# Performance work log

Measured on AMD Instinct MI355X. Metric: run time of the kernel, lower is better.

The kernel has to match this reference:

```python
import jax, jax.numpy as jnp
import numpy as np

B, S, ENC, DEC, ATT = 32, 2048, 1024, 1024, 1024


def setup_inputs() -> dict:
    key = jax.random.key(0)
    k1, k2, k3, k4, k5, k6 = jax.random.split(key, 6)
    sc = lambda fan_in: 1.0 / np.sqrt(fan_in)
    return {
        "encoder_hidden_states": jax.random.normal(k1, (B, S, ENC), dtype=jnp.float32),
        "decoder_hidden_state": jax.random.normal(k2, (B, 1, DEC), dtype=jnp.float32),
        # nn.Linear stores weight as [out, in]; we keep [in, out] for x @ W
        "U_a": jax.random.uniform(k3, (ENC, ATT), jnp.float32, -sc(ENC), sc(ENC)),
        "W_a": jax.random.uniform(k4, (DEC, ATT), jnp.float32, -sc(DEC), sc(DEC)),
        "v_t": jax.random.uniform(k5, (ATT, 1), jnp.float32, -sc(ATT), sc(ATT)),
        "ffn": jax.random.uniform(k6, (ENC + DEC, DEC), jnp.float32, -sc(ENC + DEC), sc(ENC + DEC)),
    }


def reference(encoder_hidden_states, decoder_hidden_state, U_a, W_a, v_t, ffn):
    # additive (Bahdanau) attention
    u = jnp.einsum('bse,ea->bsa', encoder_hidden_states, U_a)      # [B,S,A]
    w = jnp.einsum('bqd,da->bqa', decoder_hidden_state, W_a)       # [B,1,A]
    e = jnp.tanh(w + u) @ v_t                                      # [B,S,1]
    align = jax.nn.softmax(e, axis=1)                              # softmax over seq
    # context = alignment^T @ encoder_states  -> [B,1,E]
    context = jnp.einsum('bsq,bse->bqe', align, encoder_hidden_states)
    cat = jnp.concatenate([decoder_hidden_state, context], axis=-1)  # [B,1,D+E]
    output = jnp.tanh(cat @ ffn)                                     # [B,1,D]
    return (output, context)
```

## Files before the change

### kernel.cpp

```cpp
#include <hip/hip_runtime.h>
#include <hip/hip_bf16.h>
#include <cstdint>
#include <cstddef>

#define B_  32
#define S_  2048
#define E_  1024
#define A_  1024
#define D_  1024
#define M_TOT (B_ * S_)

typedef __attribute__((ext_vector_type(8))) __bf16 bf16x8;
typedef __attribute__((ext_vector_type(4))) float  f32x4;

__device__ __forceinline__ float fast_tanh(float x) {
    float cx = fminf(fmaxf(x, -15.f), 15.f);
    float e2 = __expf(2.f * cx);
    return 1.f - 2.f / (e2 + 1.f);
}

__device__ __forceinline__ bf16x8 cvt8(const float* __restrict__ p) {
    float4 f0 = *(const float4*)p;
    float4 f1 = *(const float4*)(p + 4);
    bf16x8 r;
    r[0] = (__bf16)f0.x; r[1] = (__bf16)f0.y; r[2] = (__bf16)f0.z; r[3] = (__bf16)f0.w;
    r[4] = (__bf16)f1.x; r[5] = (__bf16)f1.y; r[6] = (__bf16)f1.z; r[7] = (__bf16)f1.w;
    return r;
}

typedef __attribute__((address_space(3))) uint32_t lds_u32_t;
typedef __attribute__((address_space(1))) const uint32_t gbl_u32_t;
__device__ __forceinline__ void async_ld16(const void* g, void* l) {
    __builtin_amdgcn_global_load_lds((gbl_u32_t*)g,
                                     (lds_u32_t*)(uint32_t)(uintptr_t)l,
                                     16, 0, 0);
}

__global__ __launch_bounds__(256) void k_convert_enc(const float* __restrict__ enc,
                                                     __bf16* __restrict__ xb) {
    size_t idx = ((size_t)blockIdx.x * 256 + threadIdx.x) * 8;
    *(bf16x8*)(xb + idx) = cvt8(enc + idx);
}

__global__ __launch_bounds__(256) void k_trans_U(const float* __restrict__ Ua,
                                                 __bf16* __restrict__ Ut) {
    __shared__ float tile[64][65];
    int bid = blockIdx.x;
    int k0 = (bid >> 4) * 64, n0 = (bid & 15) * 64;
    int t = threadIdx.x;
    int r = t >> 6, c = t & 63;
    #pragma unroll
    for (int i = 0; i < 16; ++i)
        tile[i * 4 + r][c] = Ua[(size_t)(k0 + i * 4 + r) * 1024 + n0 + c];
    __syncthreads();
    #pragma unroll
    for (int i = 0; i < 16; ++i)
        Ut[(size_t)(n0 + i * 4 + r) * 1024 + k0 + c] = (__bf16)tile[c][i * 4 + r];
}

__global__ __launch_bounds__(256) void k_w_part(const float* __restrict__ dec,
                                                const float* __restrict__ Wa,
                                                float* __restrict__ w_part) {
    int bid = blockIdx.x;
    int ac = bid & 3, b = (bid >> 2) & 31, kc = bid >> 7;
    int a = ac * 256 + threadIdx.x;
    int k0 = kc * 128;
    float acc = 0.f;
    #pragma unroll 8
    for (int k = 0; k < 128; ++k)
        acc += dec[b * 1024 + k0 + k] * Wa[(size_t)(k0 + k) * 1024 + a];
    w_part[kc * 32768 + b * 1024 + a] = acc;
}

template <bool USE_XB>
__global__ __launch_bounds__(256) void k_gemm_e(
        const float* __restrict__ enc, const __bf16* __restrict__ Xb,
        const __bf16* __restrict__ Ut, const float* __restrict__ w_part,
        const float* __restrict__ v, float* __restrict__ e_part) {
    __shared__ __bf16 lX[2][128 * 32];
    __shared__ __bf16 lU[2][128 * 32];
    __shared__ float  e_lds[2][128];

    const int t = threadIdx.x;
    const int bid = blockIdx.x;
    const int xcd = bid & 7;
    const int j_  = bid >> 3;
    const int m_tile = xcd * 64 + (j_ >> 3);
    const int n_tile = j_ & 7;
    const int m0 = m_tile * 128;
    const int n0 = n_tile * 128;
    const int wave = t >> 6;
    const int lane = t & 63;
    const int q = lane >> 4;
    const int c = lane & 15;
    const int wm = (wave >> 1) * 64;
    const int wn = (wave & 1) * 64;

    f32x4 acc[4][4];
    #pragma unroll
    for (int i = 0; i < 4; ++i)
        #pragma unroll
        for (int j = 0; j < 4; ++j)
            #pragma unroll
            for (int r = 0; r < 4; ++r) acc[i][j][r] = 0.f;

    const int lrow = lane >> 2;
    const int lcol = (lane & 3) * 8;
    const int xrow = wave * 32;

    if (USE_XB) {
        const __bf16* gxb = Xb + (size_t)(m0 + xrow + lrow) * 1024 + lcol;
        const __bf16* gub = Ut + (size_t)(n0 + xrow + lrow) * 1024 + lcol;

        auto stage = [&](int kk, int bsel) {
            async_ld16(gxb + kk,             &lX[bsel][xrow * 32]);
            async_ld16(gxb + kk + 16 * 1024, &lX[bsel][(xrow + 16) * 32]);
            async_ld16(gub + kk,             &lU[bsel][xrow * 32]);
            async_ld16(gub + kk + 16 * 1024, &lU[bsel][(xrow + 16) * 32]);
        };
        auto compute = [&](int bsel) {
            bf16x8 af[4], bfr[4];
            #pragma unroll
            for (int i = 0; i < 4; ++i)
                af[i] = *(const bf16x8*)(&lX[bsel][(wm + i * 16 + c) * 32 + q * 8]);
            #pragma unroll
            for (int j = 0; j < 4; ++j)
                bfr[j] = *(const bf16x8*)(&lU[bsel][(wn + j * 16 + c) * 32 + q * 8]);
            #pragma unroll
            for (int i = 0; i < 4; ++i)
                #pragma unroll
                for (int j = 0; j < 4; ++j)
                    acc[i][j] = __builtin_amdgcn_mfma_f32_16x16x32_bf16(af[i], bfr[j], acc[i][j], 0, 0, 0);
        };

        stage(0, 0);
        __syncthreads();
        for (int kk = 0; kk < 1024; kk += 64) {
            if (kk + 32 < 1024) stage(kk + 32, 1);
            compute(0);
            __syncthreads();
            if (kk + 64 < 1024) stage(kk + 64, 0);
            compute(1);
            __syncthreads();
        }
    } else {
        const int srow = t >> 2;
        const int scol = (t & 3) * 8;
        for (int kk = 0; kk < 1024; kk += 32) {
            __syncthreads();
            const float* s0 = enc + (size_t)(m0 + srow) * 1024 + kk + scol;
            *(bf16x8*)(&lX[0][srow * 32])        = cvt8(s0);
            *(bf16x8*)(&lX[0][(srow + 64) * 32]) = cvt8(s0 + (size_t)64 * 1024);
            const __bf16* u0 = Ut + (size_t)(n0 + srow) * 1024 + kk + scol;
            *(int4*)(&lU[0][srow * 32])        = *(const int4*)u0;
            *(int4*)(&lU[0][(srow + 64) * 32]) = *(const int4*)(u0 + 64 * 1024);
            __syncthreads();
            bf16x8 af[4], bfr[4];
            #pragma unroll
            for (int i = 0; i < 4; ++i)
                af[i] = *(const bf16x8*)(&lX[0][(wm + i * 16 + c) * 32 + q * 8]);
            #pragma unroll
            for (int j = 0; j < 4; ++j)
                bfr[j] = *(const bf16x8*)(&lU[0][(wn + j * 16 + c) * 32 + q * 8]);
            #pragma unroll
            for (int i = 0; i < 4; ++i)
                #pragma unroll
                for (int j = 0; j < 4; ++j)
                    acc[i][j] = __builtin_amdgcn_mfma_f32_16x16x32_bf16(af[i], bfr[j], acc[i][j], 0, 0, 0);
        }
    }

    const int b_idx = m0 >> 11;
    float wv[4], vv[4];
    #pragma unroll
    for (int j = 0; j < 4; ++j) {
        int col = n0 + wn + j * 16 + c;
        float s = 0.f;
        #pragma unroll
        for (int p = 0; p < 8; ++p) s += w_part[p * 32768 + b_idx * 1024 + col];
        wv[j] = s;
        vv[j] = v[col];
    }
    #pragma unroll
    for (int i = 0; i < 4; ++i) {
        float s0 = 0.f, s1 = 0.f, s2 = 0.f, s3 = 0.f;
        #pragma unroll
        for (int j = 0; j < 4; ++j) {
            s0 += fast_tanh(wv[j] + acc[i][j][0]) * vv[j];
            s1 += fast_tanh(wv[j] + acc[i][j][1]) * vv[j];
            s2 += fast_tanh(wv[j] + acc[i][j][2]) * vv[j];
            s3 += fast_tanh(wv[j] + acc[i][j][3]) * vv[j];
        }
        #pragma unroll
        for (int off = 1; off < 16; off <<= 1) {
            s0 += __shfl_xor(s0, off, 16);
            s1 += __shfl_xor(s1, off, 16);
            s2 += __shfl_xor(s2, off, 16);
            s3 += __shfl_xor(s3, off, 16);
        }
        if (c == 0) {
            int row = wm + i * 16 + q * 4;
            e_lds[wave & 1][row + 0] = s0;
            e_lds[wave & 1][row + 1] = s1;
            e_lds[wave & 1][row + 2] = s2;
            e_lds[wave & 1][row + 3] = s3;
        }
    }
    __syncthreads();
    if (t < 128)
        e_part[(size_t)n_tile * M_TOT + m0 + t] = e_lds[0][t] + e_lds[1][t];
}

__global__ __launch_bounds__(256) void k_softmax(const float* __restrict__ ep,
                                                 float* __restrict__ al) {
    int b = blockIdx.x, t = threadIdx.x;
    float ev[8];
    #pragma unroll
    for (int i = 0; i < 8; ++i) {
        int s = i * 256 + t;
        float x = 0.f;
        #pragma unroll
        for (int p = 0; p < 8; ++p) x += ep[p * M_TOT + b * 2048 + s];
        ev[i] = x;
    }
    float mx = ev[0];
    #pragma unroll
    for (int i = 1; i < 8; ++i) mx = fmaxf(mx, ev[i]);
    #pragma unroll
    for (int off = 1; off < 64; off <<= 1) mx = fmaxf(mx, __shfl_xor(mx, off, 64));
    __shared__ float redm[4];
    if ((t & 63) == 0) redm[t >> 6] = mx;
    __syncthreads();
    mx = fmaxf(fmaxf(redm[0], redm[1]), fmaxf(redm[2], redm[3]));

    float ex[8], sm = 0.f;
    #pragma unroll
    for (int i = 0; i < 8; ++i) { ex[i] = __expf(ev[i] - mx); sm += ex[i]; }
    #pragma unroll
    for (int off = 1; off < 64; off <<= 1) sm += __shfl_xor(sm, off, 64);
    __shared__ float reds[4];
    if ((t & 63) == 0) reds[t >> 6] = sm;
    __syncthreads();
    sm = reds[0] + reds[1] + reds[2] + reds[3];
    float inv = 1.f / sm;
    #pragma unroll
    for (int i = 0; i < 8; ++i) al[b * 2048 + i * 256 + t] = ex[i] * inv;
}

template <bool USE_XB>
__global__ __launch_bounds__(256) void k_ctx(const float* __restrict__ enc,
                                             const __bf16* __restrict__ Xb,
                                             const float* __restrict__ al,
                                             float* __restrict__ ctx_part) {
    int b  = blockIdx.x >> 5;
    int sc = blockIdx.x & 31;
    int t  = threadIdx.x;
    int sh = t >> 7;
    int e8 = (t & 127) * 8;
    float acc[8];
    #pragma unroll
    for (int r = 0; r < 8; ++r) acc[r] = 0.f;
    int rbase = sc * 64 + sh * 32;
    for (int i = 0; i < 32; i += 4) {
        #pragma unroll
        for (int u = 0; u < 4; ++u) {
            int s = rbase + i + u;
            float a = al[b * 2048 + s];
            if (USE_XB) {
                bf16x8 x = *(const bf16x8*)(Xb + (size_t)(b * 2048 + s) * 1024 + e8);
                #pragma unroll
                for (int r = 0; r < 8; ++r) acc[r] += a * (float)x[r];
            } else {
                const float* xp = enc + (size_t)(b * 2048 + s) * 1024 + e8;
                float4 x0 = *(const float4*)xp;
                float4 x1 = *(const float4*)(xp + 4);
                acc[0] += a * x0.x; acc[1] += a * x0.y; acc[2] += a * x0.z; acc[3] += a * x0.w;
                acc[4] += a * x1.x; acc[5] += a * x1.y; acc[6] += a * x1.z; acc[7] += a * x1.w;
            }
        }
    }
    float* o = ctx_part + ((size_t)(sc * 2 + sh) * 32 + b) * 1024 + e8;
    float4 r0; r0.x = acc[0]; r0.y = acc[1]; r0.z = acc[2]; r0.w = acc[3];
    float4 r1; r1.x = acc[4]; r1.y = acc[5]; r1.z = acc[6]; r1.w = acc[7];
    *(float4*)o = r0;
    *(float4*)(o + 4) = r1;
}

__global__ __launch_bounds__(256) void k_ctx_sum(const float* __restrict__ ctx_part,
                                                 float* __restrict__ ctx,
                                                 float* __restrict__ out) {
    int idx = blockIdx.x * 256 + threadIdx.x;
    float s = 0.f;
    #pragma unroll
    for (int p = 0; p < 64; ++p) s += ctx_part[(size_t)p * 32768 + idx];
    ctx[idx] = s;
    out[32768 + idx] = s;
}

__global__ __launch_bounds__(256) void k_out_part(const float* __restrict__ dec,
                                                  const float* __restrict__ ctx,
                                                  const float* __restrict__ ffn,
                                                  float* __restrict__ out_part) {
    int bid = blockIdx.x;
    int b = bid & 31, kc = bid >> 5;
    int t = threadIdx.x;
    __shared__ float catl[256];
    int i0 = kc * 256;
    catl[t] = (i0 < 1024) ? dec[b * 1024 + i0 + t] : ctx[b * 1024 + i0 - 1024 + t];
    __syncthreads();
    float a0 = 0.f, a1 = 0.f, a2 = 0.f, a3 = 0.f;
    #pragma unroll 4
    for (int i = 0; i < 256; ++i) {
        float cv = catl[i];
        const float* fr = ffn + (size_t)(i0 + i) * 1024;
        a0 += cv * fr[t];
        a1 += cv * fr[t + 256];
        a2 += cv * fr[t + 512];
        a3 += cv * fr[t + 768];
    }
    float* o = out_part + ((size_t)kc * 32 + b) * 1024;
    o[t] = a0; o[t + 256] = a1; o[t + 512] = a2; o[t + 768] = a3;
}

__global__ __launch_bounds__(256) void k_out_final(const float* __restrict__ out_part,
                                                   float* __restrict__ out) {
    int idx = blockIdx.x * 256 + threadIdx.x;
    float s = 0.f;
    #pragma unroll
    for (int p = 0; p < 8; ++p) s += out_part[(size_t)p * 32768 + idx];
    out[idx] = fast_tanh(s);
}

extern "C" void kernel_launch(void* const* d_in, const int* in_sizes, int n_in,
                              void* d_out, int out_size, void* d_ws, size_t ws_size,
                              hipStream_t stream) {
    const float* enc = (const float*)d_in[0];
    const float* dec = (const float*)d_in[1];
    const float* Ua  = (const float*)d_in[2];
    const float* Wa  = (const float*)d_in[3];
    const float* vt  = (const float*)d_in[4];
    const float* ffn = (const float*)d_in[5];
    float* out = (float*)d_out;

    char* ws = (char*)d_ws;
    size_t off = 0;
    __bf16* Ut       = (__bf16*)(ws + off); off += (size_t)A_ * E_ * 2;
    float*  e_part   = (float*)(ws + off);  off += (size_t)8 * M_TOT * 4;
    float*  al       = (float*)(ws + off);  off += (size_t)M_TOT * 4;
    float*  w_part   = (float*)(ws + off);  off += (size_t)8 * B_ * 1024 * 4;
    float*  ctx_part = (float*)(ws + off);  off += (size_t)64 * B_ * 1024 * 4;
    float*  ctx      = (float*)(ws + off);  off += (size_t)B_ * 1024 * 4;
    float*  out_part = (float*)(ws + off);  off += (size_t)8 * B_ * 1024 * 4;
    off = (off + 255) & ~(size_t)255;
    __bf16* Xb       = (__bf16*)(ws + off);
    bool use_xb = (ws_size >= off + (size_t)M_TOT * E_ * 2);

    if (use_xb)
        k_convert_enc<<<(M_TOT * E_) / (256 * 8), 256, 0, stream>>>(enc, Xb);
    k_trans_U<<<256, 256, 0, stream>>>(Ua, Ut);
    k_w_part<<<1024, 256, 0, stream>>>(dec, Wa, w_part);
    if (use_xb)
        k_gemm_e<true><<<4096, 256, 0, stream>>>(enc, Xb, Ut, w_part, vt, e_part);
    else
        k_gemm_e<false><<<4096, 256, 0, stream>>>(enc, Xb, Ut, w_part, vt, e_part);
    k_softmax<<<B_, 256, 0, stream>>>(e_part, al);
    if (use_xb)
        k_ctx<true><<<B_ * 32, 256, 0, stream>>>(enc, Xb, al, ctx_part);
    else
        k_ctx<false><<<B_ * 32, 256, 0, stream>>>(enc, Xb, al, ctx_part);
    k_ctx_sum<<<(B_ * 1024) / 256, 256, 0, stream>>>(ctx_part, ctx, out);
    k_out_part<<<256, 256, 0, stream>>>(dec, ctx, ffn, out_part);
    k_out_final<<<(B_ * 1024) / 256, 256, 0, stream>>>(out_part, out);
}
```

Before: 701.4 us.

## Fuse encoder fp32-to-bf16 conversion into GEMM loads and merge tail kernels

Drops the separate pass that converted the whole encoder tensor to bf16. The GEMM now loads fp32 encoder tiles into registers, converts them and writes them to LDS inside its double-buffered loop, while U still arrives through async global-to-LDS loads. The context kernel reads fp32 directly and writes 32 partials. The ctx sum, output GEMV and tanh are merged into one final kernel. This removes a full write and reread of a 128MB bf16 copy and several launches, in exchange for twice the A-operand global traffic in the GEMM and register-staged loads.

```diff
diff --git a/kernel.cpp b/kernel.cpp
--- a/kernel.cpp
+++ b/kernel.cpp
@@ -19,9 +19,7 @@
     return 1.f - 2.f / (e2 + 1.f);
 }
 
-__device__ __forceinline__ bf16x8 cvt8(const float* __restrict__ p) {
-    float4 f0 = *(const float4*)p;
-    float4 f1 = *(const float4*)(p + 4);
+__device__ __forceinline__ bf16x8 pack8(float4 f0, float4 f1) {
     bf16x8 r;
     r[0] = (__bf16)f0.x; r[1] = (__bf16)f0.y; r[2] = (__bf16)f0.z; r[3] = (__bf16)f0.w;
     r[4] = (__bf16)f1.x; r[5] = (__bf16)f1.y; r[6] = (__bf16)f1.z; r[7] = (__bf16)f1.w;
@@ -34,12 +32,6 @@
     __builtin_amdgcn_global_load_lds((gbl_u32_t*)g,
                                      (lds_u32_t*)(uint32_t)(uintptr_t)l,
                                      16, 0, 0);
-}
-
-__global__ __launch_bounds__(256) void k_convert_enc(const float* __restrict__ enc,
-                                                     __bf16* __restrict__ xb) {
-    size_t idx = ((size_t)blockIdx.x * 256 + threadIdx.x) * 8;
-    *(bf16x8*)(xb + idx) = cvt8(enc + idx);
 }
 
 __global__ __launch_bounds__(256) void k_trans_U(const float* __restrict__ Ua,
@@ -72,11 +64,10 @@
     w_part[kc * 32768 + b * 1024 + a] = acc;
 }
 
-template <bool USE_XB>
 __global__ __launch_bounds__(256) void k_gemm_e(
-        const float* __restrict__ enc, const __bf16* __restrict__ Xb,
-        const __bf16* __restrict__ Ut, const float* __restrict__ w_part,
-        const float* __restrict__ v, float* __restrict__ e_part) {
+        const float* __restrict__ enc, const __bf16* __restrict__ Ut,
+        const float* __restrict__ w_part, const float* __restrict__ v,
+        float* __restrict__ e_part) {
     __shared__ __bf16 lX[2][128 * 32];
     __shared__ __bf16 lU[2][128 * 32];
     __shared__ float  e_lds[2][128];
@@ -108,66 +99,54 @@
     const int lcol = (lane & 3) * 8;
     const int xrow = wave * 32;
 
-    if (USE_XB) {
-        const __bf16* gxb = Xb + (size_t)(m0 + xrow + lrow) * 1024 + lcol;
-        const __bf16* gub = Ut + (size_t)(n0 + xrow + lrow) * 1024 + lcol;
-
-        auto stage = [&](int kk, int bsel) {
-            async_ld16(gxb + kk,             &lX[bsel][xrow * 32]);
-            async_ld16(gxb + kk + 16 * 1024, &lX[bsel][(xrow + 16) * 32]);
-            async_ld16(gub + kk,             &lU[bsel][xrow * 32]);
-            async_ld16(gub + kk + 16 * 1024, &lU[bsel][(xrow + 16) * 32]);
-        };
-        auto compute = [&](int bsel) {
-            bf16x8 af[4], bfr[4];
-            #pragma unroll
-            for (int i = 0; i < 4; ++i)
-                af[i] = *(const bf16x8*)(&lX[bsel][(wm + i * 16 + c) * 32 + q * 8]);
+    const float*  gxa = enc + (size_t)(m0 + xrow + lrow) * 1024 + lcol;
+    const __bf16* gub = Ut  + (size_t)(n0 + xrow + lrow) * 1024 + lcol;
+
+    float4 f0, f1, f2, f3;
+    auto loadA = [&](int kk) {
+        const float* p = gxa + kk;
+        f0 = *(const float4*)p;
+        f1 = *(const float4*)(p + 4);
+        f2 = *(const float4*)(p + 16 * 1024);
+        f3 = *(const float4*)(p + 16 * 1024 + 4);
+    };
+    auto writeA = [&](int bsel) {
+        *(bf16x8*)(&lX[bsel][(xrow + lrow) * 32 + lcol])      = pack8(f0, f1);
+        *(bf16x8*)(&lX[bsel][(xrow + 16 + lrow) * 32 + lcol]) = pack8(f2, f3);
+    };
+    auto stageB = [&](int kk, int bsel) {
+        async_ld16(gub + kk,             &lU[bsel][xrow * 32]);
+        async_ld16(gub + kk + 16 * 1024, &lU[bsel][(xrow + 16) * 32]);
+    };
+    auto compute = [&](int bsel) {
+        bf16x8 af[4], bfr[4];
+        #pragma unroll
+        for (int i = 0; i < 4; ++i)
+            af[i] = *(const bf16x8*)(&lX[bsel][(wm + i * 16 + c) * 32 + q * 8]);
+        #pragma unroll
+        for (int j = 0; j < 4; ++j)
+            bfr[j] = *(const bf16x8*)(&lU[bsel][(wn + j * 16 + c) * 32 + q * 8]);
+        #pragma unroll
+        for (int i = 0; i < 4; ++i)
             #pragma unroll
             for (int j = 0; j < 4; ++j)
-                bfr[j] = *(const bf16x8*)(&lU[bsel][(wn + j * 16 + c) * 32 + q * 8]);
-            #pragma unroll
-            for (int i = 0; i < 4; ++i)
-                #pragma unroll
-                for (int j = 0; j < 4; ++j)
-                    acc[i][j] = __builtin_amdgcn_mfma_f32_16x16x32_bf16(af[i], bfr[j], acc[i][j], 0, 0, 0);
-        };
-
-        stage(0, 0);
+                acc[i][j] = __builtin_amdgcn_mfma_f32_16x16x32_bf16(af[i], bfr[j], acc[i][j], 0, 0, 0);
+    };
+
+    loadA(0);
+    stageB(0, 0);
+    writeA(0);
+    __syncthreads();
+
+    for (int kk = 0; kk < 1024; kk += 64) {
+        if (kk + 32 < 1024) { loadA(kk + 32); stageB(kk + 32, 1); }
+        compute(0);
+        if (kk + 32 < 1024) writeA(1);
         __syncthreads();
-        for (int kk = 0; kk < 1024; kk += 64) {
-            if (kk + 32 < 1024) stage(kk + 32, 1);
-            compute(0);
-            __syncthreads();
-            if (kk + 64 < 1024) stage(kk + 64, 0);
-            compute(1);
-            __syncthreads();
-        }
-    } else {
-        const int srow = t >> 2;
-        const int scol = (t & 3) * 8;
-        for (int kk = 0; kk < 1024; kk += 32) {
-            __syncthreads();
-            const float* s0 = enc + (size_t)(m0 + srow) * 1024 + kk + scol;
-            *(bf16x8*)(&lX[0][srow * 32])        = cvt8(s0);
-            *(bf16x8*)(&lX[0][(srow + 64) * 32]) = cvt8(s0 + (size_t)64 * 1024);
-            const __bf16* u0 = Ut + (size_t)(n0 + srow) * 1024 + kk + scol;
-            *(int4*)(&lU[0][srow * 32])        = *(const int4*)u0;
-            *(int4*)(&lU[0][(srow + 64) * 32]) = *(const int4*)(u0 + 64 * 1024);
-            __syncthreads();
-            bf16x8 af[4], bfr[4];
-            #pragma unroll
-            for (int i = 0; i < 4; ++i)
-                af[i] = *(const bf16x8*)(&lX[0][(wm + i * 16 + c) * 32 + q * 8]);
-            #pragma unroll
-            for (int j = 0; j < 4; ++j)
-                bfr[j] = *(const bf16x8*)(&lU[0][(wn + j * 16 + c) * 32 + q * 8]);
-            #pragma unroll
-            for (int i = 0; i < 4; ++i)
-                #pragma unroll
-                for (int j = 0; j < 4; ++j)
-                    acc[i][j] = __builtin_amdgcn_mfma_f32_16x16x32_bf16(af[i], bfr[j], acc[i][j], 0, 0, 0);
-        }
+        if (kk + 64 < 1024) { loadA(kk + 64); stageB(kk + 64, 0); }
+        compute(1);
+        if (kk + 64 < 1024) writeA(0);
+        __syncthreads();
     }
 
     const int b_idx = m0 >> 11;
@@ -247,88 +226,68 @@
     for (int i = 0; i < 8; ++i) al[b * 2048 + i * 256 + t] = ex[i] * inv;
 }
 
-template <bool USE_XB>
 __global__ __launch_bounds__(256) void k_ctx(const float* __restrict__ enc,
-                                             const __bf16* __restrict__ Xb,
                                              const float* __restrict__ al,
                                              float* __restrict__ ctx_part) {
     int b  = blockIdx.x >> 5;
     int sc = blockIdx.x & 31;
     int t  = threadIdx.x;
-    int sh = t >> 7;
-    int e8 = (t & 127) * 8;
-    float acc[8];
-    #pragma unroll
-    for (int r = 0; r < 8; ++r) acc[r] = 0.f;
-    int rbase = sc * 64 + sh * 32;
-    for (int i = 0; i < 32; i += 4) {
+    int e4 = t * 4;
+    float ax = 0.f, ay = 0.f, az = 0.f, aw = 0.f;
+    int sbase = sc * 64;
+    for (int i = 0; i < 64; i += 4) {
         #pragma unroll
         for (int u = 0; u < 4; ++u) {
-            int s = rbase + i + u;
+            int s = sbase + i + u;
             float a = al[b * 2048 + s];
-            if (USE_XB) {
-                bf16x8 x = *(const bf16x8*)(Xb + (size_t)(b * 2048 + s) * 1024 + e8);
-                #pragma unroll
-                for (int r = 0; r < 8; ++r) acc[r] += a * (float)x[r];
-            } else {
-                const float* xp = enc + (size_t)(b * 2048 + s) * 1024 + e8;
-                float4 x0 = *(const float4*)xp;
-                float4 x1 = *(const float4*)(xp + 4);
-                acc[0] += a * x0.x; acc[1] += a * x0.y; acc[2] += a * x0.z; acc[3] += a * x0.w;
-                acc[4] += a * x1.x; acc[5] += a * x1.y; acc[6] += a * x1.z; acc[7] += a * x1.w;
-            }
+            float4 x = *(const float4*)(enc + (size_t)(b * 2048 + s) * 1024 + e4);
+            ax += a * x.x; ay += a * x.y; az += a * x.z; aw += a * x.w;
         }
     }
-    float* o = ctx_part + ((size_t)(sc * 2 + sh) * 32 + b) * 1024 + e8;
-    float4 r0; r0.x = acc[0]; r0.y = acc[1]; r0.z = acc[2]; r0.w = acc[3];
-    float4 r1; r1.x = acc[4]; r1.y = acc[5]; r1.z = acc[6]; r1.w = acc[7];
-    *(float4*)o = r0;
-    *(float4*)(o + 4) = r1;
-}
-
-__global__ __launch_bounds__(256) void k_ctx_sum(const float* __restrict__ ctx_part,
-                                                 float* __restrict__ ctx,
-                                                 float* __restrict__ out) {
-    int idx = blockIdx.x * 256 + threadIdx.x;
-    float s = 0.f;
-    #pragma unroll
-    for (int p = 0; p < 64; ++p) s += ctx_part[(size_t)p * 32768 + idx];
-    ctx[idx] = s;
-    out[32768 + idx] = s;
-}
-
-__global__ __launch_bounds__(256) void k_out_part(const float* __restrict__ dec,
-                                                  const float* __restrict__ ctx,
-                                                  const float* __restrict__ ffn,
-                                                  float* __restrict__ out_part) {
-    int bid = blockIdx.x;
-    int b = bid & 31, kc = bid >> 5;
-    int t = threadIdx.x;
-    __shared__ float catl[256];
-    int i0 = kc * 256;
-    catl[t] = (i0 < 1024) ? dec[b * 1024 + i0 + t] : ctx[b * 1024 + i0 - 1024 + t];
-    __syncthreads();
-    float a0 = 0.f, a1 = 0.f, a2 = 0.f, a3 = 0.f;
-    #pragma unroll 4
-    for (int i = 0; i < 256; ++i) {
-        float cv = catl[i];
-        const float* fr = ffn + (size_t)(i0 + i) * 1024;
-        a0 += cv * fr[t];
-        a1 += cv * fr[t + 256];
-        a2 += cv * fr[t + 512];
-        a3 += cv * fr[t + 768];
-    }
-    float* o = out_part + ((size_t)kc * 32 + b) * 1024;
-    o[t] = a0; o[t + 256] = a1; o[t + 512] = a2; o[t + 768] = a3;
-}
-
-__global__ __launch_bounds__(256) void k_out_final(const float* __restrict__ out_part,
-                                                   float* __restrict__ out) {
-    int idx = blockIdx.x * 256 + threadIdx.x;
-    float s = 0.f;
-    #pragma unroll
-    for (int p = 0; p < 8; ++p) s += out_part[(size_t)p * 32768 + idx];
-    out[idx] = fast_tanh(s);
+    float4 r; r.x = ax; r.y = ay; r.z = az; r.w = aw;
+    *(float4*)(ctx_part + ((size_t)sc * 32 + b) * 1024 + e4) = r;
+}
+
+__global__ __launch_bounds__(256) void k_final(const float* __restrict__ dec,
+                                               const float* __restrict__ ffn,
+                                               const float* __restrict__ ctx_part,
+                                               float* __restrict__ out) {
+    int b  = blockIdx.x >> 4;
+    int dc = blockIdx.x & 15;
+    int t  = threadIdx.x;
+    __shared__ float cat[2048];
+    __shared__ float red[4][64];
+
+    #pragma unroll
+    for (int r = 0; r < 4; ++r) {
+        int e = r * 256 + t;
+        cat[e] = dec[b * 1024 + e];
+        float s = 0.f;
+        #pragma unroll
+        for (int p = 0; p < 32; ++p) s += ctx_part[((size_t)p * 32 + b) * 1024 + e];
+        cat[1024 + e] = s;
+        if (dc == 0) out[32768 + b * 1024 + e] = s;
+    }
+    __syncthreads();
+
+    int dl = t & 63, ic = t >> 6;
+    int d  = dc * 64 + dl;
+    float acc = 0.f;
+    int i0 = ic * 512;
+    for (int i = 0; i < 512; i += 4) {
+        float4 cv = *(const float4*)(cat + i0 + i);
+        const float* fr = ffn + (size_t)(i0 + i) * 1024 + d;
+        acc += cv.x * fr[0];
+        acc += cv.y * fr[1024];
+        acc += cv.z * fr[2048];
+        acc += cv.w * fr[3072];
+    }
+    red[ic][dl] = acc;
+    __syncthreads();
+    if (t < 64) {
+        float s = red[0][t] + red[1][t] + red[2][t] + red[3][t];
+        out[b * 1024 + dc * 64 + t] = fast_tanh(s);
+    }
 }
 
 extern "C" void kernel_launch(void* const* d_in, const int* in_sizes, int n_in,
@@ -348,27 +307,12 @@
     float*  e_part   = (float*)(ws + off);  off += (size_t)8 * M_TOT * 4;
     float*  al       = (float*)(ws + off);  off += (size_t)M_TOT * 4;
     float*  w_part   = (float*)(ws + off);  off += (size_t)8 * B_ * 1024 * 4;
-    float*  ctx_part = (float*)(ws + off);  off += (size_t)64 * B_ * 1024 * 4;
-    float*  ctx      = (float*)(ws + off);  off += (size_t)B_ * 1024 * 4;
-    float*  out_part = (float*)(ws + off);  off += (size_t)8 * B_ * 1024 * 4;
-    off = (off + 255) & ~(size_t)255;
-    __bf16* Xb       = (__bf16*)(ws + off);
-    bool use_xb = (ws_size >= off + (size_t)M_TOT * E_ * 2);
-
-    if (use_xb)
-        k_convert_enc<<<(M_TOT * E_) / (256 * 8), 256, 0, stream>>>(enc, Xb);
+    float*  ctx_part = (float*)(ws + off);  off += (size_t)32 * B_ * 1024 * 4;
+
     k_trans_U<<<256, 256, 0, stream>>>(Ua, Ut);
     k_w_part<<<1024, 256, 0, stream>>>(dec, Wa, w_part);
-    if (use_xb)
-        k_gemm_e<true><<<4096, 256, 0, stream>>>(enc, Xb, Ut, w_part, vt, e_part);
-    else
-        k_gemm_e<false><<<4096, 256, 0, stream>>>(enc, Xb, Ut, w_part, vt, e_part);
+    k_gemm_e<<<4096, 256, 0, stream>>>(enc, Ut, w_part, vt, e_part);
     k_softmax<<<B_, 256, 0, stream>>>(e_part, al);
-    if (use_xb)
-        k_ctx<true><<<B_ * 32, 256, 0, stream>>>(enc, Xb, al, ctx_part);
-    else
-        k_ctx<false><<<B_ * 32, 256, 0, stream>>>(enc, Xb, al, ctx_part);
-    k_ctx_sum<<<(B_ * 1024) / 256, 256, 0, stream>>>(ctx_part, ctx, out);
-    k_out_part<<<256, 256, 0, stream>>>(dec, ctx, ffn, out_part);
-    k_out_final<<<(B_ * 1024) / 256, 256, 0, stream>>>(out_part, out);
-}
+    k_ctx<<<B_ * 32, 256, 0, stream>>>(enc, al, ctx_part);
+    k_final<<<B_ * 16, 256, 0, stream>>>(dec, ffn, ctx_part, out);
+}
```

New measurement: 696.2 us. Within noise of the previous version (-0.7%).
